# Optimization experiments

Hardware: AMD Instinct MI355X
Metric: run time of the kernel (lower is better)

Reference implementation:

```python
import jax, jax.numpy as jnp
import numpy as np

B, H, W, C = 16, 128, 128, 192
WS, SHIFT, HEADS = 8, 4, 6
N = WS * WS
HD = C // HEADS
SCALE = HD ** -0.5
EPS = 1e-5


def _rel_pos_index():
    coords = np.stack(np.meshgrid(np.arange(WS), np.arange(WS), indexing='ij')).reshape(2, -1)
    rel = (coords[:, :, None] - coords[:, None, :]).transpose(1, 2, 0)
    rel[..., 0] += WS - 1
    rel[..., 1] += WS - 1
    rel[..., 0] *= 2 * WS - 1
    return rel.sum(-1)  # [N, N] int


def _attn_mask():
    img = np.zeros((H, W), np.float32)
    sl = [(0, H - WS), (H - WS, H - SHIFT), (H - SHIFT, H)]
    cnt = 0
    for h0, h1 in sl:
        for w0, w1 in sl:
            img[h0:h1, w0:w1] = cnt
            cnt += 1
    mw = img.reshape(H // WS, WS, W // WS, WS).transpose(0, 2, 1, 3).reshape(-1, N)
    am = mw[:, None, :] - mw[:, :, None]
    return np.where(am != 0, np.float32(-100.0), np.float32(0.0))  # [nW, N, N]


REL_IDX = jnp.asarray(_rel_pos_index())
ATTN_MASK = jnp.asarray(_attn_mask())


def _ln(x, g, b):
    mu = x.mean(-1, keepdims=True)
    var = ((x - mu) ** 2).mean(-1, keepdims=True)
    return (x - mu) * jax.lax.rsqrt(var + EPS) * g + b


def setup_inputs() -> dict:
    key = jax.random.key(0)
    ks = jax.random.split(key, 12)
    d = {
        'x': jax.random.normal(ks[0], (B, H * W, C), jnp.float32),
        'norm1_g': jnp.ones((C,), jnp.float32),
        'norm1_b': jnp.zeros((C,), jnp.float32),
        'qkv_w': jax.random.normal(ks[1], (3 * C, C), jnp.float32) * 0.02,
        'qkv_b': jnp.zeros((3 * C,), jnp.float32),
        'proj_w': jax.random.normal(ks[2], (C, C), jnp.float32) * 0.02,
        'proj_b': jnp.zeros((C,), jnp.float32),
        'rpb_table': jax.random.normal(ks[3], ((2 * WS - 1) ** 2, HEADS), jnp.float32) * 0.02,
        'norm2_g': jnp.ones((C,), jnp.float32),
        'norm2_b': jnp.zeros((C,), jnp.float32),
        'fc1_w': jax.random.normal(ks[4], (4 * C, C), jnp.float32) * 0.02,
        'fc1_b': jnp.zeros((4 * C,), jnp.float32),
        'fc2_w': jax.random.normal(ks[5], (C, 4 * C), jnp.float32) * 0.02,
        'fc2_b': jnp.zeros((C,), jnp.float32),
    }
    return d


def reference(x, norm1_g, norm1_b, qkv_w, qkv_b, proj_w, proj_b, rpb_table,
              norm2_g, norm2_b, fc1_w, fc1_b, fc2_w, fc2_b):
    shortcut = x
    h = _ln(x, norm1_g, norm1_b).reshape(B, H, W, C)
    # cyclic shift (SW-MSA)
    h = jnp.roll(h, shift=(-SHIFT, -SHIFT), axis=(1, 2))
    # window partition -> [B*nW, N, C]
    h = h.reshape(B, H // WS, WS, W // WS, WS, C).transpose(0, 1, 3, 2, 4, 5)
    xw = h.reshape(-1, N, C)
    Bw = xw.shape[0]
    nW = (H // WS) * (W // WS)
    # qkv projection
    qkv = xw @ qkv_w.T + qkv_b  # [Bw, N, 3C]
    qkv = qkv.reshape(Bw, N, 3, HEADS, HD).transpose(2, 0, 3, 1, 4)
    q, k, v = qkv[0], qkv[1], qkv[2]  # [Bw, HEADS, N, HD]
    attn = jnp.einsum('bhnd,bhmd->bhnm', q * SCALE, k)
    # relative position bias gather: [N*N, HEADS] -> [HEADS, N, N]
    bias = rpb_table[REL_IDX.reshape(-1)].reshape(N, N, HEADS).transpose(2, 0, 1)
    attn = attn + bias[None]
    # shift mask add per-window
    attn = attn.reshape(B, nW, HEADS, N, N) + ATTN_MASK[None, :, None, :, :]
    attn = jax.nn.softmax(attn.reshape(Bw, HEADS, N, N), axis=-1)
    out = jnp.einsum('bhnm,bhmd->bhnd', attn, v)
    out = out.transpose(0, 2, 1, 3).reshape(Bw, N, C)
    out = out @ proj_w.T + proj_b
    # window reverse
    out = out.reshape(B, H // WS, W // WS, WS, WS, C).transpose(0, 1, 3, 2, 4, 5)
    out = out.reshape(B, H, W, C)
    out = jnp.roll(out, shift=(SHIFT, SHIFT), axis=(1, 2)).reshape(B, H * W, C)
    h = shortcut + out
    # MLP with residual
    m = _ln(h, norm2_g, norm2_b)
    m = jax.nn.gelu(m @ fc1_w.T + fc1_b, approximate=False)
    m = m @ fc2_w.T + fc2_b
    return h + m
```

## Files before the change

### kernel.cpp

```cpp
#include <hip/hip_runtime.h>
#include <hip/hip_bf16.h>

typedef __bf16 bf16;
typedef __bf16 bf16x4 __attribute__((ext_vector_type(4)));
typedef __bf16 bf16x8 __attribute__((ext_vector_type(8)));
typedef float f32x4 __attribute__((ext_vector_type(4)));

#define MFMA16(a, b, c) __builtin_amdgcn_mfma_f32_16x16x32_bf16(a, b, c, 0, 0, 0)

#define SCALE_Q 0.17677669529663687f

__global__ __launch_bounds__(256) void prep_kernel(
    const float* __restrict__ qkv_w, const float* __restrict__ proj_w,
    const float* __restrict__ fc1_w, const float* __restrict__ fc2_w,
    const float* __restrict__ rpb,
    bf16* __restrict__ wqkv, bf16* __restrict__ wproj,
    bf16* __restrict__ wfc1, bf16* __restrict__ wfc2,
    float* __restrict__ bias_full) {
  const int i = blockIdx.x * 256 + threadIdx.x;
  if (i < 110592) wqkv[i] = (bf16)qkv_w[i];
  if (i < 36864)  wproj[i] = (bf16)proj_w[i];
  if (i < 147456) { wfc1[i] = (bf16)fc1_w[i]; wfc2[i] = (bf16)fc2_w[i]; }
  if (i < 24576) {
    const int head = i >> 12;
    const int row = (i >> 6) & 63, col = i & 63;
    const int idx = ((row >> 3) - (col >> 3) + 7) * 15 + ((row & 7) - (col & 7) + 7);
    bias_full[i] = rpb[idx * 6 + head];
  }
}

__device__ __forceinline__ int region8(int tok, int wy, int wx) {
  const int gh = wy * 8 + (tok >> 3), gw = wx * 8 + (tok & 7);
  const int rs = (gh < 120) ? 0 : ((gh < 124) ? 1 : 2);
  const int cs = (gw < 120) ? 0 : ((gw < 124) ? 1 : 2);
  return rs * 3 + cs;
}

__global__ __launch_bounds__(384, 1) void swin_block_kernel(
    const float* __restrict__ x,
    const float* __restrict__ n1g, const float* __restrict__ n1b,
    const bf16* __restrict__ wqkv, const float* __restrict__ qkv_b,
    const bf16* __restrict__ wproj, const float* __restrict__ proj_b,
    const float* __restrict__ bias_full,
    const float* __restrict__ n2g, const float* __restrict__ n2b,
    const bf16* __restrict__ wfc1, const float* __restrict__ fc1_b,
    const bf16* __restrict__ wfc2, const float* __restrict__ fc2_b,
    float* __restrict__ out) {
  __shared__ __align__(16) char smem[76800];
  bf16*  a_s  = (bf16*)(smem);
  bf16*  q_s  = (bf16*)(smem);
  bf16*  k_s  = (bf16*)(smem + 24576);
  bf16*  vT_s = (bf16*)(smem + 49152);
  bf16*  ao_s = (bf16*)(smem);
  bf16*  m_s  = (bf16*)(smem);
  bf16*  g_s  = (bf16*)(smem + 25600);
  float* red_s = (float*)(smem + 51200);

  const int lane = threadIdx.x & 63, waveid = threadIdx.x >> 6;
  const int c = lane & 15, quad = lane >> 4;
  const int window = blockIdx.x;
  const int bi = window >> 8, w_in = window & 255;
  const int wy = w_in >> 4, wx = w_in & 15;
  const f32x4 fzero = {0.f, 0.f, 0.f, 0.f};

  auto p_ptr = [&](int head, int row, int colbyte) -> bf16* {
    int off = (row << 7) + colbyte;
    off ^= (row & 7) << 4;
    return (bf16*)(smem + (head << 13) + off);
  };

  for (int it = 0; it < 11; it++) {
    const int n = waveid * 11 + it;
    if (n < 64) {
      const int oh = (wy * 8 + (n >> 3) + 4) & 127;
      const int ow = (wx * 8 + (n & 7) + 4) & 127;
      const float* xr = x + (size_t)(bi * 16384 + oh * 128 + ow) * 192;
      float v0 = xr[lane], v1 = xr[lane + 64], v2 = xr[lane + 128];
      float s = v0 + v1 + v2;
      float s2 = v0 * v0 + v1 * v1 + v2 * v2;
#pragma unroll
      for (int off = 1; off < 64; off <<= 1) {
        s += __shfl_xor(s, off);
        s2 += __shfl_xor(s2, off);
      }
      const float mu = s * (1.f / 192.f);
      const float rinv = rsqrtf(s2 * (1.f / 192.f) - mu * mu + 1e-5f);
      a_s[n * 200 + lane]       = (bf16)((v0 - mu) * rinv * n1g[lane]       + n1b[lane]);
      a_s[n * 200 + lane + 64]  = (bf16)((v1 - mu) * rinv * n1g[lane + 64]  + n1b[lane + 64]);
      a_s[n * 200 + lane + 128] = (bf16)((v2 - mu) * rinv * n1g[lane + 128] + n1b[lane + 128]);
    }
  }
  __syncthreads();

  {
    f32x4 acc[4][6];
#pragma unroll
    for (int i = 0; i < 4; i++)
#pragma unroll
      for (int j = 0; j < 6; j++) acc[i][j] = fzero;
#pragma unroll
    for (int ks = 0; ks < 6; ks++) {
      bf16x8 a[4], w[6];
#pragma unroll
      for (int i = 0; i < 4; i++)
        a[i] = *(const bf16x8*)&a_s[(16 * i + c) * 200 + ks * 32 + quad * 8];
#pragma unroll
      for (int j = 0; j < 6; j++)
        w[j] = *(const bf16x8*)(wqkv +
            (size_t)(waveid * 96 + 16 * j + c) * 192 + ks * 32 + quad * 8);
#pragma unroll
      for (int i = 0; i < 4; i++)
#pragma unroll
        for (int j = 0; j < 6; j++) acc[i][j] = MFMA16(a[i], w[j], acc[i][j]);
    }
    __syncthreads();
    const int which = waveid >> 1;
    if (which == 2) {
#pragma unroll
      for (int j = 0; j < 6; j++) {
        const int col = waveid * 96 + 16 * j + c;
        const int sub = col - 384;
        const int head = sub >> 5, d = sub & 31;
        const float bias = qkv_b[col];
#pragma unroll
        for (int i = 0; i < 4; i++) {
          bf16x4 pk;
#pragma unroll
          for (int r = 0; r < 4; r++) pk[r] = (bf16)(acc[i][j][r] + bias);
          *(bf16x4*)&vT_s[head * 2304 + d * 72 + 16 * i + 4 * quad] = pk;
        }
      }
    } else {
#pragma unroll
      for (int j = 0; j < 6; j++) {
        const int col = waveid * 96 + 16 * j + c;
        const int sub = col - which * 192;
        const int head = sub >> 5, d = sub & 31;
        const float bias = qkv_b[col];
#pragma unroll
        for (int i = 0; i < 4; i++)
#pragma unroll
          for (int r = 0; r < 4; r++) {
            const int n = 16 * i + 4 * quad + r;
            const float val = acc[i][j][r] + bias;
            if (which == 0) q_s[head * 2048 + n * 32 + d] = (bf16)(val * SCALE_Q);
            else            k_s[head * 2048 + n * 32 + d] = (bf16)val;
          }
      }
    }
  }
  __syncthreads();

  f32x4 o[4][2];
  {
    const int head = waveid;
    bf16x8 aq[4], bk[4];
#pragma unroll
    for (int i = 0; i < 4; i++)
      aq[i] = *(const bf16x8*)&q_s[head * 2048 + (16 * i + c) * 32 + quad * 8];
#pragma unroll
    for (int j = 0; j < 4; j++)
      bk[j] = *(const bf16x8*)&k_s[head * 2048 + (16 * j + c) * 32 + quad * 8];
    __syncthreads();

    f32x4 s[4][4];
#pragma unroll
    for (int i = 0; i < 4; i++)
#pragma unroll
      for (int j = 0; j < 4; j++) s[i][j] = fzero;
#pragma unroll
    for (int i = 0; i < 4; i++)
#pragma unroll
      for (int j = 0; j < 4; j++) s[i][j] = MFMA16(aq[i], bk[j], s[i][j]);

    const float* bfp = bias_full + head * 4096;
#pragma unroll
    for (int i = 0; i < 4; i++)
#pragma unroll
      for (int r = 0; r < 4; r++) {
        const int row = 16 * i + 4 * quad + r;
#pragma unroll
        for (int j = 0; j < 4; j++) s[i][j][r] += bfp[row * 64 + 16 * j + c];
      }

    if (wy == 15 || wx == 15) {
      int creg[4];
#pragma unroll
      for (int j = 0; j < 4; j++) creg[j] = region8(16 * j + c, wy, wx);
#pragma unroll
      for (int i = 0; i < 4; i++)
#pragma unroll
        for (int r = 0; r < 4; r++) {
          const int rreg = region8(16 * i + 4 * quad + r, wy, wx);
#pragma unroll
          for (int j = 0; j < 4; j++)
            if (rreg != creg[j]) s[i][j][r] -= 100.f;
        }
    }

#pragma unroll
    for (int i = 0; i < 4; i++)
#pragma unroll
      for (int r = 0; r < 4; r++) {
        float mx = fmaxf(fmaxf(s[i][0][r], s[i][1][r]), fmaxf(s[i][2][r], s[i][3][r]));
#pragma unroll
        for (int off = 1; off < 16; off <<= 1) mx = fmaxf(mx, __shfl_xor(mx, off));
        float sum = 0.f;
#pragma unroll
        for (int j = 0; j < 4; j++) {
          const float p = __expf(s[i][j][r] - mx);
          s[i][j][r] = p;
          sum += p;
        }
#pragma unroll
        for (int off = 1; off < 16; off <<= 1) sum += __shfl_xor(sum, off);
        const float inv = 1.f / sum;
        const int row = 16 * i + 4 * quad + r;
#pragma unroll
        for (int j = 0; j < 4; j++)
          *p_ptr(head, row, (16 * j + c) * 2) = (bf16)(s[i][j][r] * inv);
      }

#pragma unroll
    for (int i = 0; i < 4; i++)
#pragma unroll
      for (int tn = 0; tn < 2; tn++) o[i][tn] = fzero;
#pragma unroll
    for (int ks = 0; ks < 2; ks++) {
      bf16x8 ap[4], bv[2];
#pragma unroll
      for (int i = 0; i < 4; i++)
        ap[i] = *(const bf16x8*)p_ptr(head, 16 * i + c, ks * 64 + quad * 16);
#pragma unroll
      for (int tn = 0; tn < 2; tn++)
        bv[tn] = *(const bf16x8*)&vT_s[head * 2304 + (16 * tn + c) * 72 + ks * 32 + quad * 8];
#pragma unroll
      for (int i = 0; i < 4; i++)
#pragma unroll
        for (int tn = 0; tn < 2; tn++) o[i][tn] = MFMA16(ap[i], bv[tn], o[i][tn]);
    }
  }
  __syncthreads();

#pragma unroll
  for (int i = 0; i < 4; i++)
#pragma unroll
    for (int tn = 0; tn < 2; tn++)
#pragma unroll
      for (int r = 0; r < 4; r++)
        ao_s[(16 * i + 4 * quad + r) * 200 + waveid * 32 + 16 * tn + c] = (bf16)o[i][tn][r];
  __syncthreads();

  float hv[4][2][4];
  {
    f32x4 acc[4][2];
#pragma unroll
    for (int i = 0; i < 4; i++)
#pragma unroll
      for (int j = 0; j < 2; j++) acc[i][j] = fzero;
#pragma unroll
    for (int ks = 0; ks < 6; ks++) {
      bf16x8 a[4], w[2];
#pragma unroll
      for (int i = 0; i < 4; i++)
        a[i] = *(const bf16x8*)&ao_s[(16 * i + c) * 200 + ks * 32 + quad * 8];
#pragma unroll
      for (int j = 0; j < 2; j++)
        w[j] = *(const bf16x8*)(wproj +
            (size_t)(waveid * 32 + 16 * j + c) * 192 + ks * 32 + quad * 8);
#pragma unroll
      for (int i = 0; i < 4; i++)
#pragma unroll
        for (int j = 0; j < 2; j++) acc[i][j] = MFMA16(a[i], w[j], acc[i][j]);
    }
#pragma unroll
    for (int i = 0; i < 4; i++)
#pragma unroll
      for (int r = 0; r < 4; r++) {
        const int n = 16 * i + 4 * quad + r;
        const int oh = (wy * 8 + (n >> 3) + 4) & 127;
        const int ow = (wx * 8 + (n & 7) + 4) & 127;
        const size_t base = (size_t)(bi * 16384 + oh * 128 + ow) * 192;
        const float* xr = x + base;
        float* orow = out + base;
#pragma unroll
        for (int j = 0; j < 2; j++) {
          const int col = waveid * 32 + 16 * j + c;
          const float h = acc[i][j][r] + proj_b[col] + xr[col];
          hv[i][j][r] = h;
          orow[col] = h;
        }
      }
  }

#pragma unroll
  for (int i = 0; i < 4; i++)
#pragma unroll
    for (int r = 0; r < 4; r++) {
      float s1 = hv[i][0][r] + hv[i][1][r];
      float s2 = hv[i][0][r] * hv[i][0][r] + hv[i][1][r] * hv[i][1][r];
#pragma unroll
      for (int off = 1; off < 16; off <<= 1) {
        s1 += __shfl_xor(s1, off);
        s2 += __shfl_xor(s2, off);
      }
      if (c == 0) {
        const int n = 16 * i + 4 * quad + r;
        red_s[n * 16 + waveid] = s1;
        red_s[n * 16 + 8 + waveid] = s2;
      }
    }
  __syncthreads();

  {
    const int col0 = waveid * 32 + c, col1 = col0 + 16;
    const float g0 = n2g[col0], b0 = n2b[col0];
    const float g1 = n2g[col1], b1 = n2b[col1];
#pragma unroll
    for (int i = 0; i < 4; i++)
#pragma unroll
      for (int r = 0; r < 4; r++) {
        const int n = 16 * i + 4 * quad + r;
        const f32x4 lo = *(const f32x4*)&red_s[n * 16 + 0];
        const f32x4 hi = *(const f32x4*)&red_s[n * 16 + 4];
        const f32x4 qlo = *(const f32x4*)&red_s[n * 16 + 8];
        const f32x4 qhi = *(const f32x4*)&red_s[n * 16 + 12];
        const float s1 = lo[0] + lo[1] + lo[2] + lo[3] + hi[0] + hi[1];
        const float s2 = qlo[0] + qlo[1] + qlo[2] + qlo[3] + qhi[0] + qhi[1];
        const float mu = s1 * (1.f / 192.f);
        const float rinv = rsqrtf(s2 * (1.f / 192.f) - mu * mu + 1e-5f);
        m_s[n * 200 + col0] = (bf16)((hv[i][0][r] - mu) * rinv * g0 + b0);
        m_s[n * 200 + col1] = (bf16)((hv[i][1][r] - mu) * rinv * g1 + b1);
      }
  }
  __syncthreads();

  f32x4 oacc[4][2];
#pragma unroll
  for (int i = 0; i < 4; i++)
#pragma unroll
    for (int j = 0; j < 2; j++) oacc[i][j] = fzero;

  for (int chunk = 0; chunk < 4; chunk++) {
    f32x4 gacc[4][2];
#pragma unroll
    for (int i = 0; i < 4; i++)
#pragma unroll
      for (int j = 0; j < 2; j++) gacc[i][j] = fzero;
#pragma unroll
    for (int ks = 0; ks < 6; ks++) {
      bf16x8 a[4], w[2];
#pragma unroll
      for (int i = 0; i < 4; i++)
        a[i] = *(const bf16x8*)&m_s[(16 * i + c) * 200 + ks * 32 + quad * 8];
#pragma unroll
      for (int j = 0; j < 2; j++)
        w[j] = *(const bf16x8*)(wfc1 +
            (size_t)(chunk * 192 + waveid * 32 + 16 * j + c) * 192 + ks * 32 + quad * 8);
#pragma unroll
      for (int i = 0; i < 4; i++)
#pragma unroll
        for (int j = 0; j < 2; j++) gacc[i][j] = MFMA16(a[i], w[j], gacc[i][j]);
    }
#pragma unroll
    for (int i = 0; i < 4; i++)
#pragma unroll
      for (int j = 0; j < 2; j++) {
        const int lcol = waveid * 32 + 16 * j + c;
        const float fb = fc1_b[chunk * 192 + lcol];
#pragma unroll
        for (int r = 0; r < 4; r++) {
          float val = gacc[i][j][r] + fb;
          val = 0.5f * val * (1.f + erff(val * 0.70710678118654752f));
          g_s[(16 * i + 4 * quad + r) * 200 + lcol] = (bf16)val;
        }
      }
    __syncthreads();
#pragma unroll
    for (int ks = 0; ks < 6; ks++) {
      bf16x8 a[4], w[2];
#pragma unroll
      for (int i = 0; i < 4; i++)
        a[i] = *(const bf16x8*)&g_s[(16 * i + c) * 200 + ks * 32 + quad * 8];
#pragma unroll
      for (int j = 0; j < 2; j++)
        w[j] = *(const bf16x8*)(wfc2 +
            (size_t)(waveid * 32 + 16 * j + c) * 768 + chunk * 192 + ks * 32 + quad * 8);
#pragma unroll
      for (int i = 0; i < 4; i++)
#pragma unroll
        for (int j = 0; j < 2; j++) oacc[i][j] = MFMA16(a[i], w[j], oacc[i][j]);
    }
    __syncthreads();
  }

#pragma unroll
  for (int i = 0; i < 4; i++)
#pragma unroll
    for (int r = 0; r < 4; r++) {
      const int n = 16 * i + 4 * quad + r;
      const int oh = (wy * 8 + (n >> 3) + 4) & 127;
      const int ow = (wx * 8 + (n & 7) + 4) & 127;
      float* orow = out + (size_t)(bi * 16384 + oh * 128 + ow) * 192;
#pragma unroll
      for (int j = 0; j < 2; j++) {
        const int col = waveid * 32 + 16 * j + c;
        const float h = orow[col];
        orow[col] = oacc[i][j][r] + fc2_b[col] + h;
      }
    }
}

extern "C" void kernel_launch(void* const* d_in, const int* in_sizes, int n_in,
                              void* d_out, int out_size, void* d_ws, size_t ws_size,
                              hipStream_t stream) {
  const float* x      = (const float*)d_in[0];
  const float* n1g    = (const float*)d_in[1];
  const float* n1b    = (const float*)d_in[2];
  const float* qkv_w  = (const float*)d_in[3];
  const float* qkv_b  = (const float*)d_in[4];
  const float* proj_w = (const float*)d_in[5];
  const float* proj_b = (const float*)d_in[6];
  const float* rpb    = (const float*)d_in[7];
  const float* n2g    = (const float*)d_in[8];
  const float* n2b    = (const float*)d_in[9];
  const float* fc1_w  = (const float*)d_in[10];
  const float* fc1_b  = (const float*)d_in[11];
  const float* fc2_w  = (const float*)d_in[12];
  const float* fc2_b  = (const float*)d_in[13];

  char* ws = (char*)d_ws;
  float* biasf = (float*)(ws);
  bf16*  wqkv  = (bf16*)(ws + 98304);
  bf16*  wproj = (bf16*)(ws + 98304 + 221184);
  bf16*  wfc1  = (bf16*)(ws + 98304 + 221184 + 73728);
  bf16*  wfc2  = (bf16*)(ws + 98304 + 221184 + 73728 + 294912);

  prep_kernel<<<576, 256, 0, stream>>>(qkv_w, proj_w, fc1_w, fc2_w, rpb,
                                       wqkv, wproj, wfc1, wfc2, biasf);
  swin_block_kernel<<<4096, 384, 0, stream>>>(
      x, n1g, n1b, wqkv, qkv_b, wproj, proj_b, biasf,
      n2g, n2b, wfc1, fc1_b, wfc2, fc2_b, (float*)d_out);
}
```

Baseline: 1.292 ms.

## Restructure QKV projection per head to cut registers and raise occupancy

The QKV GEMM is reorganised so that each wave computes q, k and v for its own head in three sequential passes. This replaces one wide 4x6 accumulator tile with 4x2 tiles. The shared-memory layout moves vT to the front, where it overlaps the consumed LayerNorm buffer, and places q/k and the probability buffer after it. Launch bounds are raised to request 3 blocks per CU, so the compiler has to cap registers to allow multiple resident blocks and latency can be hidden across windows. The risks are register spills in the unseen attention and MLP phases, and that the 76.8 KB of LDS per block may cap residency below the requested count.

```diff
diff --git a/kernel.cpp b/kernel.cpp
--- a/kernel.cpp
+++ b/kernel.cpp
@@ -36,7 +36,7 @@
   return rs * 3 + cs;
 }
 
-__global__ __launch_bounds__(384, 1) void swin_block_kernel(
+__global__ __launch_bounds__(384, 3) void swin_block_kernel(
     const float* __restrict__ x,
     const float* __restrict__ n1g, const float* __restrict__ n1b,
     const bf16* __restrict__ wqkv, const float* __restrict__ qkv_b,
@@ -48,9 +48,9 @@
     float* __restrict__ out) {
   __shared__ __align__(16) char smem[76800];
   bf16*  a_s  = (bf16*)(smem);
-  bf16*  q_s  = (bf16*)(smem);
-  bf16*  k_s  = (bf16*)(smem + 24576);
-  bf16*  vT_s = (bf16*)(smem + 49152);
+  bf16*  vT_s = (bf16*)(smem);
+  bf16*  q_s  = (bf16*)(smem + 27648);
+  bf16*  k_s  = (bf16*)(smem + 52224);
   bf16*  ao_s = (bf16*)(smem);
   bf16*  m_s  = (bf16*)(smem);
   bf16*  g_s  = (bf16*)(smem + 25600);
@@ -66,7 +66,7 @@
   auto p_ptr = [&](int head, int row, int colbyte) -> bf16* {
     int off = (row << 7) + colbyte;
     off ^= (row & 7) << 4;
-    return (bf16*)(smem + (head << 13) + off);
+    return (bf16*)(smem + 27648 + (head << 13) + off);
   };
 
   for (int it = 0; it < 11; it++) {
@@ -93,59 +93,58 @@
   __syncthreads();
 
   {
-    f32x4 acc[4][6];
-#pragma unroll
-    for (int i = 0; i < 4; i++)
-#pragma unroll
-      for (int j = 0; j < 6; j++) acc[i][j] = fzero;
-#pragma unroll
-    for (int ks = 0; ks < 6; ks++) {
-      bf16x8 a[4], w[6];
-#pragma unroll
-      for (int i = 0; i < 4; i++)
-        a[i] = *(const bf16x8*)&a_s[(16 * i + c) * 200 + ks * 32 + quad * 8];
-#pragma unroll
-      for (int j = 0; j < 6; j++)
-        w[j] = *(const bf16x8*)(wqkv +
-            (size_t)(waveid * 96 + 16 * j + c) * 192 + ks * 32 + quad * 8);
-#pragma unroll
-      for (int i = 0; i < 4; i++)
-#pragma unroll
-        for (int j = 0; j < 6; j++) acc[i][j] = MFMA16(a[i], w[j], acc[i][j]);
-    }
-    __syncthreads();
-    const int which = waveid >> 1;
-    if (which == 2) {
-#pragma unroll
-      for (int j = 0; j < 6; j++) {
-        const int col = waveid * 96 + 16 * j + c;
-        const int sub = col - 384;
-        const int head = sub >> 5, d = sub & 31;
-        const float bias = qkv_b[col];
-#pragma unroll
-        for (int i = 0; i < 4; i++) {
-          bf16x4 pk;
-#pragma unroll
-          for (int r = 0; r < 4; r++) pk[r] = (bf16)(acc[i][j][r] + bias);
-          *(bf16x4*)&vT_s[head * 2304 + d * 72 + 16 * i + 4 * quad] = pk;
-        }
-      }
-    } else {
-#pragma unroll
-      for (int j = 0; j < 6; j++) {
-        const int col = waveid * 96 + 16 * j + c;
-        const int sub = col - which * 192;
-        const int head = sub >> 5, d = sub & 31;
-        const float bias = qkv_b[col];
+    const int head = waveid;
+#pragma unroll
+    for (int which = 0; which < 3; which++) {
+      f32x4 acc[4][2];
+#pragma unroll
+      for (int i = 0; i < 4; i++)
+#pragma unroll
+        for (int j = 0; j < 2; j++) acc[i][j] = fzero;
+#pragma unroll
+      for (int ks = 0; ks < 6; ks++) {
+        bf16x8 a[4], w[2];
 #pragma unroll
         for (int i = 0; i < 4; i++)
-#pragma unroll
-          for (int r = 0; r < 4; r++) {
-            const int n = 16 * i + 4 * quad + r;
-            const float val = acc[i][j][r] + bias;
-            if (which == 0) q_s[head * 2048 + n * 32 + d] = (bf16)(val * SCALE_Q);
-            else            k_s[head * 2048 + n * 32 + d] = (bf16)val;
+          a[i] = *(const bf16x8*)&a_s[(16 * i + c) * 200 + ks * 32 + quad * 8];
+#pragma unroll
+        for (int j = 0; j < 2; j++)
+          w[j] = *(const bf16x8*)(wqkv +
+              (size_t)(which * 192 + head * 32 + 16 * j + c) * 192 + ks * 32 + quad * 8);
+#pragma unroll
+        for (int i = 0; i < 4; i++)
+#pragma unroll
+          for (int j = 0; j < 2; j++) acc[i][j] = MFMA16(a[i], w[j], acc[i][j]);
+      }
+      if (which == 2) {
+        __syncthreads();
+#pragma unroll
+        for (int j = 0; j < 2; j++) {
+          const int d = 16 * j + c;
+          const float bias = qkv_b[384 + head * 32 + d];
+#pragma unroll
+          for (int i = 0; i < 4; i++) {
+            bf16x4 pk;
+#pragma unroll
+            for (int r = 0; r < 4; r++) pk[r] = (bf16)(acc[i][j][r] + bias);
+            *(bf16x4*)&vT_s[head * 2304 + d * 72 + 16 * i + 4 * quad] = pk;
           }
+        }
+      } else {
+        bf16* dst = (which == 0) ? q_s : k_s;
+        const float mul = (which == 0) ? SCALE_Q : 1.f;
+#pragma unroll
+        for (int j = 0; j < 2; j++) {
+          const int d = 16 * j + c;
+          const float bias = qkv_b[which * 192 + head * 32 + d];
+#pragma unroll
+          for (int i = 0; i < 4; i++)
+#pragma unroll
+            for (int r = 0; r < 4; r++) {
+              const int n = 16 * i + 4 * quad + r;
+              dst[head * 2048 + n * 32 + d] = (bf16)((acc[i][j][r] + bias) * mul);
+            }
+        }
       }
     }
   }
```

Measured after the change: 1.271 ms. About the same (-1.7%).
